# Optimization experiments

Hardware: AMD Instinct MI355X
Metric: run time of the kernel (lower is better)

## Reference

```python
import jax, jax.numpy as jnp
import numpy as np

BSZ, N, E, D = 8, 1024, 49152, 256
K, ALPHA = 10, 0.1
EDGE_RATIO, NODE_RATIO = 0.8, 0.7
K_NODES = int(np.ceil(NODE_RATIO * N))  # torch_geometric topk uses ceil -> 717


def setup_inputs() -> dict:
    key = jax.random.key(0)
    ks = jax.random.split(key, 10)
    concept_hidden = jax.random.normal(ks[0], (BSZ, N, D), jnp.float32)
    head = jax.random.randint(ks[1], (BSZ, E), 0, N, jnp.int32)
    off = jax.random.randint(ks[2], (BSZ, E), 1, N, jnp.int32)
    tail = ((head + off) % N).astype(jnp.int32)  # guaranteed no self-loops
    triple_label = jnp.ones((BSZ, E), jnp.int32)  # all edges valid (no -1 padding)
    relation_hidden = jnp.zeros((BSZ, 1), jnp.float32)  # unused by the math
    concept_labels = jax.random.randint(ks[3], (BSZ, N), 0, 3, jnp.int32)
    concept_ids = jax.random.randint(ks[4], (BSZ, N), 0, 50000, jnp.int32)
    # PageRank temp (learnable param, deterministic init from alpha/K)
    t = ALPHA * (1.0 - ALPHA) ** np.arange(K + 1)
    t[-1] = (1.0 - ALPHA) ** K
    temp = jnp.asarray(t, jnp.float32)
    # GraphAttention params (heads=1)
    g = float(np.sqrt(6.0 / (D + D)))
    W_proj = jax.random.uniform(ks[5], (D, D), jnp.float32, -g, g)
    ga = float(np.sqrt(6.0 / (1 + D)))
    a_src = jax.random.uniform(ks[6], (D,), jnp.float32, -ga, ga)
    a_tgt = jax.random.uniform(ks[7], (D,), jnp.float32, -ga, ga)
    # output Linear(2D -> D)
    gl = float(np.sqrt(1.0 / (2 * D)))
    W_lin = jax.random.uniform(ks[8], (D, 2 * D), jnp.float32, -gl, gl)
    b_lin = jax.random.uniform(ks[9], (D,), jnp.float32, -gl, gl)
    return dict(concept_hidden=concept_hidden, relation_hidden=relation_hidden,
                head=head, tail=tail, triple_label=triple_label,
                concept_labels=concept_labels, concept_ids=concept_ids,
                temp=temp, W_proj=W_proj, a_src=a_src, a_tgt=a_tgt,
                W_lin=W_lin, b_lin=b_lin)


def _per_sample(x, h, t, labels, ids, temp, W_proj, a_src, a_tgt, W_lin, b_lin):
    # ---- PageRank (gcn_norm with added self-loops, aggr='add' into tail) ----
    sl = jnp.arange(N, dtype=jnp.int32)
    hs = jnp.concatenate([h, sl])
    ts = jnp.concatenate([t, sl])
    deg = jax.ops.segment_sum(jnp.ones(E + N, x.dtype), ts, num_segments=N)
    dinv = jnp.where(deg > 0, jax.lax.rsqrt(deg), 0.0)
    norm = dinv[hs] * dinv[ts]  # [E+N]

    def step(xk, gamma):
        xk = jax.ops.segment_sum(norm[:, None] * xk[hs], ts, num_segments=N)
        return xk, gamma * xk

    _, contribs = jax.lax.scan(step, x, temp[1:])  # K steps
    x_cut = temp[0] * x + contribs.sum(0)  # [N, D]

    # ---- edge attention (GAT-style scoring, sigmoid) ----
    proj = x_cut @ W_proj.T                       # [N, D] (heads=1)
    s_src = proj @ a_src                          # [N]
    s_tgt = proj @ a_tgt                          # [N]
    attn = jax.nn.sigmoid(s_src[h] + s_tgt[t])    # [E]

    # ---- symmetrize + coalesce(mean), done densely ----
    rows = jnp.concatenate([h, t])
    cols = jnp.concatenate([t, h])
    vals = jnp.concatenate([attn, attn])
    S = jnp.zeros((N, N), x.dtype).at[rows, cols].add(vals)
    Cn = jnp.zeros((N, N), x.dtype).at[rows, cols].add(1.0)
    valid = Cn > 0
    A = jnp.where(valid, S / jnp.maximum(Cn, 1.0), 0.0)  # coalesced mean adjacency

    # ---- np.percentile(attn, 20) with linear interpolation over valid edges ----
    sv = jnp.sort(jnp.where(valid, A, jnp.inf).reshape(-1))  # valid values first
    M = valid.sum()
    pos = (1.0 - EDGE_RATIO) * (M.astype(x.dtype) - 1.0)
    lo = jnp.floor(pos).astype(jnp.int32)
    frac = pos - lo.astype(x.dtype)
    hi = jnp.minimum(lo + 1, M - 1)  # stays within the finite (valid) prefix
    cut = sv[lo] + frac * (sv[hi] - sv[lo])

    A_cut = jnp.where(valid & (A >= cut), A, 0.0)  # edges below percentile zeroed

    # ---- node scoring: scatter_add of attn*x[src] into dst == A_cut^T @ x ----
    out = A_cut.T @ x                              # [N, D]
    score = jnp.abs(out).sum(1) + 1e-7             # [N]
    _, perm = jax.lax.top_k(score, K_NODES)

    pooled = A_cut[perm] @ x                       # [k, D]
    hcat = jnp.concatenate([x[perm], pooled], axis=-1)  # [k, 2D]
    h_new = hcat @ W_lin.T + b_lin                 # [k, D]
    return h_new, labels[perm], ids[perm]


def reference(concept_hidden, relation_hidden, head, tail, triple_label,
              concept_labels, concept_ids, temp, W_proj, a_src, a_tgt,
              W_lin, b_lin):
    f = jax.vmap(_per_sample,
                 in_axes=(0, 0, 0, 0, 0, None, None, None, None, None, None))
    return f(concept_hidden, head, tail, concept_labels, concept_ids,
             temp, W_proj, a_src, a_tgt, W_lin, b_lin)
```

## Files before the change

### kernel.cpp

```cpp
#include <hip/hip_runtime.h>
#include <math.h>

#define BSZ 8
#define NN 1024
#define EE 49152
#define DD 256
#define KSTEPS 10
#define NCH 192
#define KNODES 717
#define RS 256
#define MROWS 720

typedef __attribute__((ext_vector_type(8))) short short8_t;
typedef __attribute__((ext_vector_type(4))) float f32x4;

__device__ __forceinline__ void fma4(float4& a, float w, const float4 v) {
    a.x += w * v.x; a.y += w * v.y; a.z += w * v.z; a.w += w * v.w;
}

__device__ __forceinline__ unsigned short f2bf(float f) {
    unsigned u = __float_as_uint(f);
    u = (u + 0x7fffu + ((u >> 16) & 1u)) >> 16;
    return (unsigned short)u;
}


__global__ void k_hist(const int* __restrict__ head, const int* __restrict__ tail,
                       int* __restrict__ cnt_t, int* __restrict__ cnt_h) {
    __shared__ int lt[NN];
    __shared__ int lh[NN];
    int b = blockIdx.x / NCH, ch = blockIdx.x % NCH;
    int tid = threadIdx.x;
    for (int i = tid; i < NN; i += 256) { lt[i] = 0; lh[i] = 0; }
    __syncthreads();
    int e = ch * 256 + tid;
    int h = head[b * EE + e], t = tail[b * EE + e];
    atomicAdd(&lt[t], 1);
    atomicAdd(&lh[h], 1);
    __syncthreads();
    int base = (b * NCH + ch) * NN;
    for (int i = tid; i < NN; i += 256) { cnt_t[base + i] = lt[i]; cnt_h[base + i] = lh[i]; }
}

__global__ void k_chunkscan(int* __restrict__ cnt_t, int* __restrict__ cnt_h,
                            int* __restrict__ tot_t, int* __restrict__ tot_h,
                            float* __restrict__ dinv) {
    int gid = blockIdx.x * 256 + threadIdx.x;
    int which = gid >> 13;
    int i = gid & 8191;
    int b = i >> 10, n = i & 1023;
    int* c = which ? cnt_h : cnt_t;
    int run = 0;
    for (int s = 0; s < NCH; s++) {
        int idx = (b * NCH + s) * NN + n;
        int v = c[idx];
        c[idx] = run;
        run += v;
    }
    (which ? tot_h : tot_t)[i] = run;
    if (!which) dinv[i] = 1.0f / sqrtf((float)(run + 1));
}

__global__ __launch_bounds__(1024) void k_nodescan(const int* __restrict__ tot_t,
                                                   const int* __restrict__ tot_h,
                                                   int* __restrict__ toff, int* __restrict__ hoff) {
    __shared__ int sb[NN];
    int b = blockIdx.x >> 1, which = blockIdx.x & 1;
    int tid = threadIdx.x;
    const int* tot = which ? tot_h : tot_t;
    int* off = which ? hoff : toff;
    int v = tot[b * NN + tid];
    sb[tid] = v;
    __syncthreads();
    for (int o = 1; o < NN; o <<= 1) {
        int t = (tid >= o) ? sb[tid - o] : 0;
        __syncthreads();
        sb[tid] += t;
        __syncthreads();
    }
    off[b * (NN + 1) + tid] = sb[tid] - v;
    if (tid == NN - 1) off[b * (NN + 1) + NN] = sb[tid];
}

__global__ void k_fill(const int* __restrict__ head, const int* __restrict__ tail,
                       const int* __restrict__ cnt_t, const int* __restrict__ cnt_h,
                       const int* __restrict__ toff, const int* __restrict__ hoff,
                       const float* __restrict__ dinv,
                       int* __restrict__ t_head, float* __restrict__ t_norm, int* __restrict__ t_eidx,
                       int* __restrict__ h_tail, int* __restrict__ h_eidx) {
    __shared__ int sh[256], st[256];
    int b = blockIdx.x / NCH, ch = blockIdx.x % NCH;
    int tid = threadIdx.x;
    int e = ch * 256 + tid;
    int h = head[b * EE + e], t = tail[b * EE + e];
    sh[tid] = h;
    st[tid] = t;
    __syncthreads();
    int rt = 0, rh = 0;
    for (int j = 0; j < tid; j++) {
        rt += (st[j] == t);
        rh += (sh[j] == h);
    }
    int post = toff[b * (NN + 1) + t] + cnt_t[(b * NCH + ch) * NN + t] + rt;
    t_head[b * EE + post] = h;
    t_norm[b * EE + post] = dinv[b * NN + h] * dinv[b * NN + t];
    t_eidx[b * EE + post] = e;
    int posh = hoff[b * (NN + 1) + h] + cnt_h[(b * NCH + ch) * NN + h] + rh;
    h_tail[b * EE + posh] = t;
    h_eidx[b * EE + posh] = e;
}

__global__ __launch_bounds__(256) void k_prstep(const float* __restrict__ src, float* __restrict__ dst,
                         float* __restrict__ xacc, const float* __restrict__ temp,
                         const int* __restrict__ toff, const int* __restrict__ t_head,
                         const float* __restrict__ t_norm, const float* __restrict__ dinv,
                         int kidx) {
    int wid = threadIdx.x >> 6, lane = threadIdx.x & 63;
    int b = blockIdx.x & 7;
    int n = (blockIdx.x >> 3) * 4 + wid;
    int g = b * NN + n;
    int o0 = __builtin_amdgcn_readfirstlane(toff[b * (NN + 1) + n]);
    int o1 = __builtin_amdgcn_readfirstlane(toff[b * (NN + 1) + n + 1]);
    int ebase = __builtin_amdgcn_readfirstlane(b * EE);
    const int* __restrict__ hp = t_head + ebase;
    const float* __restrict__ wp = t_norm + ebase;
    float dv = dinv[g];
    const float4* src4 = (const float4*)src;
    size_t r4 = (size_t)g * 64 + lane;
    size_t bb = (size_t)b * NN * 64;
    float4 sv = src4[r4];
    float sl = dv * dv;
    float4 acc;
    acc.x = sl * sv.x; acc.y = sl * sv.y; acc.z = sl * sv.z; acc.w = sl * sv.w;
    int j = o0;
    for (; j + 8 <= o1; j += 8) {
        int c0 = hp[j], c1 = hp[j + 1], c2 = hp[j + 2], c3 = hp[j + 3];
        int c4 = hp[j + 4], c5 = hp[j + 5], c6 = hp[j + 6], c7 = hp[j + 7];
        float w0 = wp[j], w1 = wp[j + 1], w2 = wp[j + 2], w3 = wp[j + 3];
        float w4 = wp[j + 4], w5 = wp[j + 5], w6 = wp[j + 6], w7 = wp[j + 7];
        float4 xa = src4[bb + (size_t)c0 * 64 + lane];
        float4 xb = src4[bb + (size_t)c1 * 64 + lane];
        float4 xc = src4[bb + (size_t)c2 * 64 + lane];
        float4 xd = src4[bb + (size_t)c3 * 64 + lane];
        float4 xe = src4[bb + (size_t)c4 * 64 + lane];
        float4 xf = src4[bb + (size_t)c5 * 64 + lane];
        float4 xg = src4[bb + (size_t)c6 * 64 + lane];
        float4 xh = src4[bb + (size_t)c7 * 64 + lane];
        fma4(acc, w0, xa); fma4(acc, w1, xb); fma4(acc, w2, xc); fma4(acc, w3, xd);
        fma4(acc, w4, xe); fma4(acc, w5, xf); fma4(acc, w6, xg); fma4(acc, w7, xh);
    }
    for (; j + 4 <= o1; j += 4) {
        int c0 = hp[j], c1 = hp[j + 1], c2 = hp[j + 2], c3 = hp[j + 3];
        float w0 = wp[j], w1 = wp[j + 1], w2 = wp[j + 2], w3 = wp[j + 3];
        float4 xa = src4[bb + (size_t)c0 * 64 + lane];
        float4 xb = src4[bb + (size_t)c1 * 64 + lane];
        float4 xc = src4[bb + (size_t)c2 * 64 + lane];
        float4 xd = src4[bb + (size_t)c3 * 64 + lane];
        fma4(acc, w0, xa); fma4(acc, w1, xb); fma4(acc, w2, xc); fma4(acc, w3, xd);
    }
    for (; j < o1; j++) {
        int c0 = hp[j];
        float w0 = wp[j];
        float4 xa = src4[bb + (size_t)c0 * 64 + lane];
        fma4(acc, w0, xa);
    }
    ((float4*)dst)[r4] = acc;
    float gm = temp[kidx + 1];
    float4 xa2;
    if (kidx == 0) {
        float t0 = temp[0];
        xa2.x = t0 * sv.x; xa2.y = t0 * sv.y; xa2.z = t0 * sv.z; xa2.w = t0 * sv.w;
    } else {
        xa2 = ((float4*)xacc)[r4];
    }
    fma4(xa2, gm, acc);
    ((float4*)xacc)[r4] = xa2;
}


__global__ void k_vsrc(const float* __restrict__ Wp, const float* __restrict__ as_,
                       const float* __restrict__ at_, float* __restrict__ vsrc,
                       float* __restrict__ vtgt) {
    int d = threadIdx.x;
    float vs = 0.f, vt = 0.f;
    for (int i = 0; i < DD; i++) {
        float w = Wp[i * DD + d];
        vs += as_[i] * w;
        vt += at_[i] * w;
    }
    vsrc[d] = vs;
    vtgt[d] = vt;
}

__global__ void k_s(const float* __restrict__ xacc, const float* __restrict__ vsrc,
                    const float* __restrict__ vtgt, float* __restrict__ ssrc,
                    float* __restrict__ stgt) {
    int g = blockIdx.x * 4 + (threadIdx.x >> 6);
    int lane = threadIdx.x & 63;
    const float4* xr = (const float4*)(xacc + (size_t)g * DD);
    float4 xv = xr[lane];
    float4 vs = ((const float4*)vsrc)[lane];
    float4 vt = ((const float4*)vtgt)[lane];
    float s1 = xv.x * vs.x + xv.y * vs.y + xv.z * vs.z + xv.w * vs.w;
    float s2 = xv.x * vt.x + xv.y * vt.y + xv.z * vt.z + xv.w * vt.w;
    for (int o = 32; o > 0; o >>= 1) {
        s1 += __shfl_down(s1, o);
        s2 += __shfl_down(s2, o);
    }
    if (lane == 0) {
        ssrc[g] = s1;
        stgt[g] = s2;
    }
}

__global__ void k_attn(const int* __restrict__ head, const int* __restrict__ tail,
                       const float* __restrict__ ssrc, const float* __restrict__ stgt,
                       float* __restrict__ attn) {
    int i = blockIdx.x * 256 + threadIdx.x;
    int b = i / EE;
    int h = head[i], t = tail[i];
    float z = ssrc[b * NN + h] + stgt[b * NN + t];
    attn[i] = 1.0f / (1.0f + expf(-z));
}


__global__ __launch_bounds__(256) void k_rowbuild(const int* __restrict__ hoff, const int* __restrict__ h_tail,
                          const int* __restrict__ h_eidx, const int* __restrict__ toff,
                          const int* __restrict__ t_head, const int* __restrict__ t_eidx,
                          const float* __restrict__ attn,
                          int* __restrict__ rcol, float* __restrict__ rval,
                          int* __restrict__ nnzrow) {
    __shared__ int cols[RS];
    __shared__ float vals[RS];
    __shared__ int first[NN];
    __shared__ int cntb[NN];
    __shared__ int rankv[NN];
    __shared__ int ssum[256];
    int g = blockIdx.x;
    int b = g >> 10, n = g & 1023;
    int tid = threadIdx.x;
    int a0 = hoff[b * (NN + 1) + n], a1 = hoff[b * (NN + 1) + n + 1];
    int c0 = toff[b * (NN + 1) + n], c1 = toff[b * (NN + 1) + n + 1];
    int kh = a1 - a0;
    int kk = kh + (c1 - c0);
    if (kk > RS) kk = RS;
    for (int i = tid; i < NN; i += 256) { first[i] = 0x7fffffff; cntb[i] = 0; }
    __syncthreads();
    if (tid < kk) {
        int c, e;
        if (tid < kh) { c = h_tail[b * EE + a0 + tid]; e = h_eidx[b * EE + a0 + tid]; }
        else          { c = t_head[b * EE + c0 + (tid - kh)]; e = t_eidx[b * EE + c0 + (tid - kh)]; }
        cols[tid] = c;
        vals[tid] = attn[b * EE + e];
        atomicMin(&first[c], tid);
        atomicAdd(&cntb[c], 1);
    }
    __syncthreads();
    int i0 = tid * 4;
    int p0 = (first[i0] != 0x7fffffff);
    int p1 = (first[i0 + 1] != 0x7fffffff);
    int p2 = (first[i0 + 2] != 0x7fffffff);
    int p3 = (first[i0 + 3] != 0x7fffffff);
    int psum = p0 + p1 + p2 + p3;
    ssum[tid] = psum;
    __syncthreads();
    for (int o = 1; o < 256; o <<= 1) {
        int t = (tid >= o) ? ssum[tid - o] : 0;
        __syncthreads();
        ssum[tid] += t;
        __syncthreads();
    }
    int run = ssum[tid] - psum;
    rankv[i0] = run;            run += p0;
    rankv[i0 + 1] = run;        run += p1;
    rankv[i0 + 2] = run;        run += p2;
    rankv[i0 + 3] = run;
    int total = ssum[255];
    __syncthreads();
    if (tid < kk) {
        int c = cols[tid];
        if (first[c] == tid) {
            int cc = cntb[c];
            float v;
            if (cc == 1) {
                v = vals[tid];
            } else {
                float s = 0.f;
                for (int j = tid; j < kk; j++)
                    if (cols[j] == c) s += vals[j];
                v = s / (float)cc;
            }
            size_t rb = ((size_t)g << 8) + rankv[c];
            rcol[rb] = c;
            rval[rb] = v;
        }
    }
    if (tid == 0) nnzrow[g] = total;
}

__global__ void k_msum(const int* __restrict__ nnzrow, int* __restrict__ Mcnt) {
    __shared__ int red[256];
    int b = blockIdx.x, tid = threadIdx.x;
    int s = nnzrow[b * NN + tid] + nnzrow[b * NN + 256 + tid] +
            nnzrow[b * NN + 512 + tid] + nnzrow[b * NN + 768 + tid];
    red[tid] = s;
    __syncthreads();
    for (int o = 128; o > 0; o >>= 1) {
        if (tid < o) red[tid] += red[tid + o];
        __syncthreads();
    }
    if (tid == 0) Mcnt[b] = red[0];
}


__global__ void k_selinit(const int* __restrict__ Mcnt, int* __restrict__ sel) {
    int b = threadIdx.x;
    if (b < BSZ) {
        int M = Mcnt[b];
        float pos = 0.2f * ((float)M - 1.0f);
        int lo = (int)floorf(pos);
        float frac = pos - (float)lo;
        sel[b * 8 + 0] = lo;
        sel[b * 8 + 1] = min(lo + 1, M - 1);
        sel[b * 8 + 2] = 0;
        sel[b * 8 + 3] = 0;
        sel[b * 8 + 4] = __float_as_int(frac);
    }
}

__global__ void k_selhist(const float* __restrict__ rv, const int* __restrict__ sel,
                          int* __restrict__ hist, int pass) {
    __shared__ int lh[512];
    int tid = threadIdx.x;
    lh[tid] = 0;
    lh[tid + 256] = 0;
    __syncthreads();
    size_t base = (size_t)blockIdx.x * 1024;
    int b = blockIdx.x >> 8;
    unsigned p0 = (unsigned)sel[b * 8 + 2];
    unsigned p1 = (unsigned)sel[b * 8 + 3];
    int shift = 24 - 8 * pass;
    for (int u = 0; u < 4; u++) {
        float a = rv[base + u * 256 + tid];
        if (a > 0.f) {
            unsigned bits = __float_as_uint(a);
            unsigned bucket = (bits >> shift) & 255u;
            if (pass == 0) {
                atomicAdd(&lh[bucket], 1);
                atomicAdd(&lh[256 + bucket], 1);
            } else {
                unsigned hibits = bits >> (shift + 8);
                if (hibits == p0) atomicAdd(&lh[bucket], 1);
                if (hibits == p1) atomicAdd(&lh[256 + bucket], 1);
            }
        }
    }
    __syncthreads();
    int v0 = lh[tid];
    if (v0) atomicAdd(&hist[(b * 2 + 0) * 256 + tid], v0);
    int v1 = lh[tid + 256];
    if (v1) atomicAdd(&hist[(b * 2 + 1) * 256 + tid], v1);
}

__global__ void k_selreduce(int* __restrict__ hist, int* __restrict__ sel) {
    __shared__ int sb[256];
    int b = blockIdx.x >> 1, ch = blockIdx.x & 1;
    int tid = threadIdx.x;
    int idx = (b * 2 + ch) * 256 + tid;
    int v = hist[idx];
    hist[idx] = 0;
    int rem = sel[b * 8 + ch];
    int pref = sel[b * 8 + 2 + ch];
    sb[tid] = v;
    __syncthreads();
    for (int o = 1; o < 256; o <<= 1) {
        int t = (tid >= o) ? sb[tid - o] : 0;
        __syncthreads();
        sb[tid] += t;
        __syncthreads();
    }
    int excl = sb[tid] - v;
    if (v > 0 && rem >= excl && rem < excl + v) {
        sel[b * 8 + ch] = rem - excl;
        sel[b * 8 + 2 + ch] = (pref << 8) | tid;
    }
}

__global__ void k_cut(const int* __restrict__ sel, float* __restrict__ cut) {
    int b = threadIdx.x;
    if (b < BSZ) {
        float v0 = __uint_as_float((unsigned)sel[b * 8 + 2]);
        float v1 = __uint_as_float((unsigned)sel[b * 8 + 3]);
        float frac = __int_as_float(sel[b * 8 + 4]);
        cut[b] = v0 + frac * (v1 - v0);
    }
}


__global__ __launch_bounds__(256) void k_outscore(const int* __restrict__ rcol, const float* __restrict__ rval,
                           const int* __restrict__ nnzrow, const float* __restrict__ x,
                           const float* __restrict__ cut, float* __restrict__ out_pr,
                           float* __restrict__ score) {
    int wid = threadIdx.x >> 6, lane = threadIdx.x & 63;
    int b = blockIdx.x & 7;
    int n = (blockIdx.x >> 3) * 4 + wid;
    int g = b * NN + n;
    float cb = cut[b];
    int nnz = __builtin_amdgcn_readfirstlane(nnzrow[g]);
    int rbase = __builtin_amdgcn_readfirstlane(g << 8);
    const int* __restrict__ cp = rcol + rbase;
    const float* __restrict__ vp = rval + rbase;
    const float4* x4 = (const float4*)x;
    size_t bb = (size_t)b * NN * 64;
    float4 acc = make_float4(0.f, 0.f, 0.f, 0.f);
    int j = 0;
    for (; j + 4 <= nnz; j += 4) {
        float a0 = vp[j], a1 = vp[j + 1], a2 = vp[j + 2], a3 = vp[j + 3];
        int c0 = cp[j], c1 = cp[j + 1], c2 = cp[j + 2], c3 = cp[j + 3];
        float4 xa = x4[bb + (size_t)c0 * 64 + lane];
        float4 xb = x4[bb + (size_t)c1 * 64 + lane];
        float4 xc = x4[bb + (size_t)c2 * 64 + lane];
        float4 xd = x4[bb + (size_t)c3 * 64 + lane];
        if (a0 >= cb) fma4(acc, a0, xa);
        if (a1 >= cb) fma4(acc, a1, xb);
        if (a2 >= cb) fma4(acc, a2, xc);
        if (a3 >= cb) fma4(acc, a3, xd);
    }
    for (; j < nnz; j++) {
        float a0 = vp[j];
        int c0 = cp[j];
        float4 xa = x4[bb + (size_t)c0 * 64 + lane];
        if (a0 >= cb) fma4(acc, a0, xa);
    }
    ((float4*)out_pr)[(size_t)g * 64 + lane] = acc;
    float4 r;
    r.x = fabsf(acc.x); r.y = fabsf(acc.y); r.z = fabsf(acc.z); r.w = fabsf(acc.w);
    for (int o = 32; o > 0; o >>= 1) {
        r.x += __shfl_down(r.x, o);
        r.y += __shfl_down(r.y, o);
        r.z += __shfl_down(r.z, o);
        r.w += __shfl_down(r.w, o);
    }
    r.x += r.z;
    r.y += r.w;
    r.x += r.y;
    if (lane == 0) score[g] = r.x + 1e-7f;
}


__global__ __launch_bounds__(1024) void k_topk(const float* __restrict__ score,
                                               const int* __restrict__ labels,
                                               const int* __restrict__ ids,
                                               int* __restrict__ perm,
                                               float* __restrict__ out_lab,
                                               float* __restrict__ out_ids) {
    __shared__ float sc[NN];
    __shared__ int idx[NN];
    int b = blockIdx.x, tid = threadIdx.x;
    sc[tid] = score[b * NN + tid];
    idx[tid] = tid;
    __syncthreads();
    for (int k = 2; k <= NN; k <<= 1) {
        for (int j = k >> 1; j > 0; j >>= 1) {
            int p = tid ^ j;
            if (p > tid) {
                float s0 = sc[tid], s1 = sc[p];
                int i0 = idx[tid], i1 = idx[p];
                bool before01 = (s0 > s1) || (s0 == s1 && i0 < i1);
                bool up = ((tid & k) == 0);
                bool sw = up ? (!before01) : before01;
                if (sw) {
                    sc[tid] = s1; sc[p] = s0;
                    idx[tid] = i1; idx[p] = i0;
                }
            }
            __syncthreads();
        }
    }
    perm[b * NN + tid] = idx[tid];
    if (tid < KNODES) {
        int p = idx[tid];
        out_lab[b * KNODES + tid] = (float)labels[b * NN + p];
        out_ids[b * KNODES + tid] = (float)ids[b * NN + p];
    }
}


__global__ void k_wbf16(const float* __restrict__ W, unsigned short* __restrict__ Wb) {
    int i = blockIdx.x * 256 + threadIdx.x;
    Wb[i] = f2bf(W[i]);
}

__global__ void k_packA(const float* __restrict__ x, const float* __restrict__ outpr,
                        const int* __restrict__ perm, unsigned short* __restrict__ A16) {
    int row = blockIdx.x;
    int b = row / MROWS, i = row - b * MROWS;
    int tid = threadIdx.x;
    size_t ob = (size_t)row * 512;
    if (i < KNODES) {
        int p = perm[b * NN + i];
        float v0 = x[((size_t)(b * NN + p)) * DD + tid];
        float v1 = outpr[((size_t)(b * NN + p)) * DD + tid];
        A16[ob + tid] = f2bf(v0);
        A16[ob + 256 + tid] = f2bf(v1);
    } else {
        A16[ob + tid] = 0;
        A16[ob + 256 + tid] = 0;
    }
}

__global__ __launch_bounds__(256) void k_hnew_mfma(const unsigned short* __restrict__ A16,
                                                   const unsigned short* __restrict__ Wb,
                                                   const float* __restrict__ b_lin,
                                                   float* __restrict__ hnew) {
    int w = blockIdx.x * 4 + (threadIdx.x >> 6);
    int lane = threadIdx.x & 63;
    int b = w / (45 * 16);
    int rem = w - b * (45 * 16);
    int mt = rem >> 4, nt = rem & 15;
    int m = lane & 15, quad = lane >> 4;
    const unsigned short* ap = A16 + ((size_t)(b * MROWS + mt * 16 + m) * 512 + quad * 8);
    const unsigned short* bp = Wb + ((size_t)(nt * 16 + m) * 512 + quad * 8);
    f32x4 acc = {0.f, 0.f, 0.f, 0.f};
#pragma unroll
    for (int s = 0; s < 16; s++) {
        short8_t av = *(const short8_t*)(ap + s * 32);
        short8_t bv = *(const short8_t*)(bp + s * 32);
        acc = __builtin_amdgcn_mfma_f32_16x16x32_bf16(av, bv, acc, 0, 0, 0);
    }
    int d = nt * 16 + m;
    float bl = b_lin[d];
#pragma unroll
    for (int r = 0; r < 4; r++) {
        int i = mt * 16 + quad * 4 + r;
        if (i < KNODES) hnew[((size_t)(b * KNODES + i)) * DD + d] = acc[r] + bl;
    }
}


extern "C" void kernel_launch(void* const* d_in, const int* in_sizes, int n_in,
                              void* d_out, int out_size, void* d_ws, size_t ws_size,
                              hipStream_t stream) {
    const float* x      = (const float*)d_in[0];
    const int*   head   = (const int*)d_in[2];
    const int*   tail   = (const int*)d_in[3];
    const int*   labels = (const int*)d_in[5];
    const int*   ids    = (const int*)d_in[6];
    const float* temp   = (const float*)d_in[7];
    const float* Wp     = (const float*)d_in[8];
    const float* asrc   = (const float*)d_in[9];
    const float* atgt   = (const float*)d_in[10];
    const float* Wl     = (const float*)d_in[11];
    const float* blin   = (const float*)d_in[12];

    float* out_h   = (float*)d_out;
    float* out_lab = out_h + (size_t)BSZ * KNODES * DD;
    float* out_ids = out_lab + (size_t)BSZ * KNODES;

    size_t o = 0;
    char* ws = (char*)d_ws;
    auto A_ = [&](size_t bytes) -> void* {
        void* p = ws + o;
        o += (bytes + 255) & ~(size_t)255;
        return p;
    };
    int*   cnt_t  = (int*)  A_((size_t)BSZ * NCH * NN * 4);
    int*   cnt_h  = (int*)  A_((size_t)BSZ * NCH * NN * 4);
    int*   tot_t  = (int*)  A_((size_t)BSZ * NN * 4);
    int*   tot_h  = (int*)  A_((size_t)BSZ * NN * 4);
    int*   toff   = (int*)  A_((size_t)BSZ * (NN + 1) * 4);
    int*   hoff   = (int*)  A_((size_t)BSZ * (NN + 1) * 4);
    float* dinv   = (float*)A_((size_t)BSZ * NN * 4);
    int*   t_head = (int*)  A_((size_t)BSZ * EE * 4);
    float* t_norm = (float*)A_((size_t)BSZ * EE * 4);
    int*   t_eidx = (int*)  A_((size_t)BSZ * EE * 4);
    int*   h_tail = (int*)  A_((size_t)BSZ * EE * 4);
    int*   h_eidx = (int*)  A_((size_t)BSZ * EE * 4);
    float* xkA    = (float*)A_((size_t)BSZ * NN * DD * 4);
    float* xkB    = (float*)A_((size_t)BSZ * NN * DD * 4);
    float* xacc   = (float*)A_((size_t)BSZ * NN * DD * 4);
    float* vsrc   = (float*)A_(DD * 4);
    float* vtgt   = (float*)A_(DD * 4);
    float* ssrc   = (float*)A_((size_t)BSZ * NN * 4);
    float* stgt   = (float*)A_((size_t)BSZ * NN * 4);
    float* attn   = (float*)A_((size_t)BSZ * EE * 4);
    int*   rcol   = (int*)  A_((size_t)BSZ * NN * RS * 4);
    float* rval   = (float*)A_((size_t)BSZ * NN * RS * 4);
    int*   nnzrow = (int*)  A_((size_t)BSZ * NN * 4);
    int*   Mcnt   = (int*)  A_(BSZ * 4);
    int*   sel    = (int*)  A_(BSZ * 8 * 4);
    int*   hist   = (int*)  A_(BSZ * 2 * 256 * 4);
    float* cutv   = (float*)A_(BSZ * 4);
    float* outpr  = (float*)A_((size_t)BSZ * NN * DD * 4);
    float* scorev = (float*)A_((size_t)BSZ * NN * 4);
    int*   perm   = (int*)  A_((size_t)BSZ * NN * 4);
    unsigned short* Wb16 = (unsigned short*)A_((size_t)DD * 512 * 2);
    unsigned short* A16  = (unsigned short*)A_((size_t)BSZ * MROWS * 512 * 2);
    if (o > ws_size) return;

    hipMemsetAsync(rval, 0, (size_t)BSZ * NN * RS * 4, stream);
    hipMemsetAsync(hist, 0, BSZ * 2 * 256 * 4, stream);

    k_wbf16<<<DD * 512 / 256, 256, 0, stream>>>(Wl, Wb16);
    k_hist<<<BSZ * NCH, 256, 0, stream>>>(head, tail, cnt_t, cnt_h);
    k_chunkscan<<<64, 256, 0, stream>>>(cnt_t, cnt_h, tot_t, tot_h, dinv);
    k_nodescan<<<16, 1024, 0, stream>>>(tot_t, tot_h, toff, hoff);
    k_fill<<<BSZ * NCH, 256, 0, stream>>>(head, tail, cnt_t, cnt_h, toff, hoff, dinv,
                                          t_head, t_norm, t_eidx, h_tail, h_eidx);
    for (int k = 0; k < KSTEPS; k++) {
        const float* src = (k == 0) ? x : ((k & 1) ? xkA : xkB);
        float* dst = (k & 1) ? xkB : xkA;
        k_prstep<<<BSZ * NN / 4, 256, 0, stream>>>(src, dst, xacc, temp, toff, t_head, t_norm, dinv, k);
    }
    k_vsrc<<<1, 256, 0, stream>>>(Wp, asrc, atgt, vsrc, vtgt);
    k_s<<<BSZ * NN / 4, 256, 0, stream>>>(xacc, vsrc, vtgt, ssrc, stgt);
    k_attn<<<BSZ * EE / 256, 256, 0, stream>>>(head, tail, ssrc, stgt, attn);
    k_rowbuild<<<BSZ * NN, 256, 0, stream>>>(hoff, h_tail, h_eidx, toff, t_head, t_eidx,
                                             attn, rcol, rval, nnzrow);
    k_msum<<<BSZ, 256, 0, stream>>>(nnzrow, Mcnt);
    k_selinit<<<1, 64, 0, stream>>>(Mcnt, sel);
    for (int p = 0; p < 4; p++) {
        k_selhist<<<BSZ * 256, 256, 0, stream>>>(rval, sel, hist, p);
        k_selreduce<<<16, 256, 0, stream>>>(hist, sel);
    }
    k_cut<<<1, 64, 0, stream>>>(sel, cutv);
    k_outscore<<<BSZ * NN / 4, 256, 0, stream>>>(rcol, rval, nnzrow, x, cutv, outpr, scorev);
    k_topk<<<BSZ, 1024, 0, stream>>>(scorev, labels, ids, perm, out_lab, out_ids);
    k_packA<<<BSZ * MROWS, 256, 0, stream>>>(x, outpr, perm, A16);
    k_hnew_mfma<<<BSZ * 45 * 16 / 4, 256, 0, stream>>>(A16, Wb16, blin, out_h);
}
```

Before: 465.3 us.

## Compact nonzero attention values for percentile selection and fold small kernels into larger launches

```diff
diff --git a/kernel.cpp b/kernel.cpp
--- a/kernel.cpp
+++ b/kernel.cpp
@@ -10,6 +10,8 @@
 #define KNODES 717
 #define RS 256
 #define MROWS 720
+#define CSTRIDE 131072
+#define SELB 64
 
 typedef __attribute__((ext_vector_type(8))) short short8_t;
 typedef __attribute__((ext_vector_type(4))) float f32x4;
@@ -26,11 +28,17 @@
 
 
 __global__ void k_hist(const int* __restrict__ head, const int* __restrict__ tail,
-                       int* __restrict__ cnt_t, int* __restrict__ cnt_h) {
+                       int* __restrict__ cnt_t, int* __restrict__ cnt_h,
+                       const float* __restrict__ Wl, unsigned short* __restrict__ Wb) {
     __shared__ int lt[NN];
     __shared__ int lh[NN];
+    int tid = threadIdx.x;
+    if (blockIdx.x >= BSZ * NCH) {
+        int i = (blockIdx.x - BSZ * NCH) * 256 + tid;
+        Wb[i] = f2bf(Wl[i]);
+        return;
+    }
     int b = blockIdx.x / NCH, ch = blockIdx.x % NCH;
-    int tid = threadIdx.x;
     for (int i = tid; i < NN; i += 256) { lt[i] = 0; lh[i] = 0; }
     __syncthreads();
     int e = ch * 256 + tid;
@@ -114,7 +122,22 @@
                          float* __restrict__ xacc, const float* __restrict__ temp,
                          const int* __restrict__ toff, const int* __restrict__ t_head,
                          const float* __restrict__ t_norm, const float* __restrict__ dinv,
-                         int kidx) {
+                         int kidx,
+                         const float* __restrict__ Wp, const float* __restrict__ as_,
+                         const float* __restrict__ at_, float* __restrict__ vsrc,
+                         float* __restrict__ vtgt) {
+    if (blockIdx.x >= BSZ * NN / 4) {
+        int d = threadIdx.x;
+        float vs = 0.f, vt = 0.f;
+        for (int i = 0; i < DD; i++) {
+            float w = Wp[i * DD + d];
+            vs += as_[i] * w;
+            vt += at_[i] * w;
+        }
+        vsrc[d] = vs;
+        vtgt[d] = vt;
+        return;
+    }
     int wid = threadIdx.x >> 6, lane = threadIdx.x & 63;
     int b = blockIdx.x & 7;
     int n = (blockIdx.x >> 3) * 4 + wid;
@@ -178,20 +201,6 @@
 }
 
 
-__global__ void k_vsrc(const float* __restrict__ Wp, const float* __restrict__ as_,
-                       const float* __restrict__ at_, float* __restrict__ vsrc,
-                       float* __restrict__ vtgt) {
-    int d = threadIdx.x;
-    float vs = 0.f, vt = 0.f;
-    for (int i = 0; i < DD; i++) {
-        float w = Wp[i * DD + d];
-        vs += as_[i] * w;
-        vt += at_[i] * w;
-    }
-    vsrc[d] = vs;
-    vtgt[d] = vt;
-}
-
 __global__ void k_s(const float* __restrict__ xacc, const float* __restrict__ vsrc,
                     const float* __restrict__ vtgt, float* __restrict__ ssrc,
                     float* __restrict__ stgt) {
@@ -229,13 +238,15 @@
                           const int* __restrict__ t_head, const int* __restrict__ t_eidx,
                           const float* __restrict__ attn,
                           int* __restrict__ rcol, float* __restrict__ rval,
-                          int* __restrict__ nnzrow) {
+                          int* __restrict__ nnzrow,
+                          float* __restrict__ cvals, int* __restrict__ ccount) {
     __shared__ int cols[RS];
     __shared__ float vals[RS];
     __shared__ int first[NN];
     __shared__ int cntb[NN];
     __shared__ int rankv[NN];
     __shared__ int ssum[256];
+    __shared__ int cbase;
     int g = blockIdx.x;
     int b = g >> 10, n = g & 1023;
     int tid = threadIdx.x;
@@ -276,6 +287,7 @@
     rankv[i0 + 2] = run;        run += p2;
     rankv[i0 + 3] = run;
     int total = ssum[255];
+    if (tid == 0) cbase = atomicAdd(&ccount[b], total);
     __syncthreads();
     if (tid < kk) {
         int c = cols[tid];
@@ -290,33 +302,21 @@
                     if (cols[j] == c) s += vals[j];
                 v = s / (float)cc;
             }
-            size_t rb = ((size_t)g << 8) + rankv[c];
+            int r = rankv[c];
+            size_t rb = ((size_t)g << 8) + r;
             rcol[rb] = c;
             rval[rb] = v;
+            cvals[(size_t)b * CSTRIDE + cbase + r] = v;
         }
     }
     if (tid == 0) nnzrow[g] = total;
 }
 
-__global__ void k_msum(const int* __restrict__ nnzrow, int* __restrict__ Mcnt) {
-    __shared__ int red[256];
-    int b = blockIdx.x, tid = threadIdx.x;
-    int s = nnzrow[b * NN + tid] + nnzrow[b * NN + 256 + tid] +
-            nnzrow[b * NN + 512 + tid] + nnzrow[b * NN + 768 + tid];
-    red[tid] = s;
-    __syncthreads();
-    for (int o = 128; o > 0; o >>= 1) {
-        if (tid < o) red[tid] += red[tid + o];
-        __syncthreads();
-    }
-    if (tid == 0) Mcnt[b] = red[0];
-}
-
-
-__global__ void k_selinit(const int* __restrict__ Mcnt, int* __restrict__ sel) {
+
+__global__ void k_selinit(const int* __restrict__ ccount, int* __restrict__ sel) {
     int b = threadIdx.x;
     if (b < BSZ) {
-        int M = Mcnt[b];
+        int M = ccount[b];
         float pos = 0.2f * ((float)M - 1.0f);
         int lo = (int)floorf(pos);
         float frac = pos - (float)lo;
@@ -328,31 +328,29 @@
     }
 }
 
-__global__ void k_selhist(const float* __restrict__ rv, const int* __restrict__ sel,
-                          int* __restrict__ hist, int pass) {
+__global__ void k_selhist(const float* __restrict__ cv, const int* __restrict__ ccount,
+                          const int* __restrict__ sel, int* __restrict__ hist, int pass) {
     __shared__ int lh[512];
     int tid = threadIdx.x;
     lh[tid] = 0;
     lh[tid + 256] = 0;
     __syncthreads();
-    size_t base = (size_t)blockIdx.x * 1024;
-    int b = blockIdx.x >> 8;
+    int b = blockIdx.x / SELB, blk = blockIdx.x % SELB;
+    int M = ccount[b];
+    const float* vp = cv + (size_t)b * CSTRIDE;
     unsigned p0 = (unsigned)sel[b * 8 + 2];
     unsigned p1 = (unsigned)sel[b * 8 + 3];
     int shift = 24 - 8 * pass;
-    for (int u = 0; u < 4; u++) {
-        float a = rv[base + u * 256 + tid];
-        if (a > 0.f) {
-            unsigned bits = __float_as_uint(a);
-            unsigned bucket = (bits >> shift) & 255u;
-            if (pass == 0) {
-                atomicAdd(&lh[bucket], 1);
-                atomicAdd(&lh[256 + bucket], 1);
-            } else {
-                unsigned hibits = bits >> (shift + 8);
-                if (hibits == p0) atomicAdd(&lh[bucket], 1);
-                if (hibits == p1) atomicAdd(&lh[256 + bucket], 1);
-            }
+    for (int i = blk * 256 + tid; i < M; i += SELB * 256) {
+        unsigned bits = __float_as_uint(vp[i]);
+        unsigned bucket = (bits >> shift) & 255u;
+        if (pass == 0) {
+            atomicAdd(&lh[bucket], 1);
+            atomicAdd(&lh[256 + bucket], 1);
+        } else {
+            unsigned hb = bits >> (shift + 8);
+            if (hb == p0) atomicAdd(&lh[bucket], 1);
+            if (hb == p1) atomicAdd(&lh[256 + bucket], 1);
         }
     }
     __syncthreads();
@@ -485,11 +483,6 @@
     }
 }
 
-
-__global__ void k_wbf16(const float* __restrict__ W, unsigned short* __restrict__ Wb) {
-    int i = blockIdx.x * 256 + threadIdx.x;
-    Wb[i] = f2bf(W[i]);
-}
 
 __global__ void k_packA(const float* __restrict__ x, const float* __restrict__ outpr,
                         const int* __restrict__ perm, unsigned short* __restrict__ A16) {
@@ -587,7 +580,8 @@
     int*   rcol   = (int*)  A_((size_t)BSZ * NN * RS * 4);
     float* rval   = (float*)A_((size_t)BSZ * NN * RS * 4);
     int*   nnzrow = (int*)  A_((size_t)BSZ * NN * 4);
-    int*   Mcnt   = (int*)  A_(BSZ * 4);
+    float* cvals  = (float*)A_((size_t)BSZ * CSTRIDE * 4);
+    int*   ccount = (int*)  A_(BSZ * 4);
     int*   sel    = (int*)  A_(BSZ * 8 * 4);
     int*   hist   = (int*)  A_(BSZ * 2 * 256 * 4);
     float* cutv   = (float*)A_(BSZ * 4);
@@ -598,11 +592,10 @@
     unsigned short* A16  = (unsigned short*)A_((size_t)BSZ * MROWS * 512 * 2);
     if (o > ws_size) return;
 
-    hipMemsetAsync(rval, 0, (size_t)BSZ * NN * RS * 4, stream);
+    hipMemsetAsync(ccount, 0, BSZ * 4, stream);
     hipMemsetAsync(hist, 0, BSZ * 2 * 256 * 4, stream);
 
-    k_wbf16<<<DD * 512 / 256, 256, 0, stream>>>(Wl, Wb16);
-    k_hist<<<BSZ * NCH, 256, 0, stream>>>(head, tail, cnt_t, cnt_h);
+    k_hist<<<BSZ * NCH + 512, 256, 0, stream>>>(head, tail, cnt_t, cnt_h, Wl, Wb16);
     k_chunkscan<<<64, 256, 0, stream>>>(cnt_t, cnt_h, tot_t, tot_h, dinv);
     k_nodescan<<<16, 1024, 0, stream>>>(tot_t, tot_h, toff, hoff);
     k_fill<<<BSZ * NCH, 256, 0, stream>>>(head, tail, cnt_t, cnt_h, toff, hoff, dinv,
@@ -610,17 +603,17 @@
     for (int k = 0; k < KSTEPS; k++) {
         const float* src = (k == 0) ? x : ((k & 1) ? xkA : xkB);
         float* dst = (k & 1) ? xkB : xkA;
-        k_prstep<<<BSZ * NN / 4, 256, 0, stream>>>(src, dst, xacc, temp, toff, t_head, t_norm, dinv, k);
-    }
-    k_vsrc<<<1, 256, 0, stream>>>(Wp, asrc, atgt, vsrc, vtgt);
+        int grid = BSZ * NN / 4 + ((k == KSTEPS - 1) ? 1 : 0);
+        k_prstep<<<grid, 256, 0, stream>>>(src, dst, xacc, temp, toff, t_head, t_norm, dinv, k,
+                                           Wp, asrc, atgt, vsrc, vtgt);
+    }
     k_s<<<BSZ * NN / 4, 256, 0, stream>>>(xacc, vsrc, vtgt, ssrc, stgt);
     k_attn<<<BSZ * EE / 256, 256, 0, stream>>>(head, tail, ssrc, stgt, attn);
     k_rowbuild<<<BSZ * NN, 256, 0, stream>>>(hoff, h_tail, h_eidx, toff, t_head, t_eidx,
-                                             attn, rcol, rval, nnzrow);
-    k_msum<<<BSZ, 256, 0, stream>>>(nnzrow, Mcnt);
-    k_selinit<<<1, 64, 0, stream>>>(Mcnt, sel);
+                                             attn, rcol, rval, nnzrow, cvals, ccount);
+    k_selinit<<<1, 64, 0, stream>>>(ccount, sel);
     for (int p = 0; p < 4; p++) {
-        k_selhist<<<BSZ * 256, 256, 0, stream>>>(rval, sel, hist, p);
+        k_selhist<<<BSZ * SELB, 256, 0, stream>>>(cvals, ccount, sel, hist, p);
         k_selreduce<<<16, 256, 0, stream>>>(hist, sel);
     }
     k_cut<<<1, 64, 0, stream>>>(sel, cutv);
```

Measured after the change: 521.2 us. 12.0% more time.
